# Kernel optimization log

Hardware: AMD Instinct MI355X
Metric: run time of the kernel (lower is better)

The kernel has to match this reference:

```python
import jax, jax.numpy as jnp
import numpy as np

B, T, N, E = 4, 12, 2000, 32000
ND, ED = 16, 8
H, D = 4, 16
G = H * D          # gat_hidden = 64
GH = 64            # gru_hidden
LN_EPS = 1e-5


def setup_inputs() -> dict:
    key = jax.random.key(0)
    ks = jax.random.split(key, 12)

    def xavier(k, shape):
        fan_in, fan_out = shape[0], shape[-1]
        lim = np.sqrt(6.0 / (fan_in + fan_out))
        return jax.random.uniform(k, shape, jnp.float32, -lim, lim)

    return {
        "node_features": jax.random.normal(ks[0], (B, T, N, ND), jnp.float32),
        "edge_features": jax.random.normal(ks[1], (B, T, E, ED), jnp.float32),
        "W_node": xavier(ks[2], (ND, G)),
        "W_edge": xavier(ks[3], (ED, G)),
        "att": xavier(ks[4], (H, 3 * D)),
        "ln_gamma": jnp.ones((G,), jnp.float32),
        "ln_beta": jnp.zeros((G,), jnp.float32),
        "W_ih": xavier(ks[5], (3 * GH, G)),
        "W_hh": xavier(ks[6], (3 * GH, GH)),
        "b_ih": jnp.zeros((3 * GH,), jnp.float32),
        "b_hh": jnp.zeros((3 * GH,), jnp.float32),
        "W_out": xavier(ks[7], (GH, 1)),
        "b_out": jnp.zeros((1,), jnp.float32),
        "edge_index": jax.random.randint(ks[8], (2, E), 0, N).astype(jnp.int64),
    }


def reference(node_features, edge_features, W_node, W_edge, att, ln_gamma,
              ln_beta, W_ih, W_hh, b_ih, b_hh, W_out, b_out, edge_index):
    Bv, Tv, Nv, _ = node_features.shape
    Ev = edge_features.shape[2]
    Hv = att.shape[0]
    Dv = att.shape[1] // 3
    Gv = Hv * Dv
    src, dst = edge_index[0], edge_index[1]
    a_dst, a_src, a_e = att[:, :Dv], att[:, Dv:2 * Dv], att[:, 2 * Dv:]

    def gat_single(x, ea):
        # x: [N, ND], ea: [E, ED]
        h = (x @ W_node).reshape(Nv, Hv, Dv)          # [N,H,D]
        e = (ea @ W_edge).reshape(Ev, Hv, Dv)          # [E,H,D]
        # score = LeakyReLU(a . [h_dst | h_src | e]) — compute per-node parts
        # at node level then gather (same math, avoids [E,H,3D] concat).
        s_d = jnp.einsum('nhd,hd->nh', h, a_dst)       # [N,H]
        s_s = jnp.einsum('nhd,hd->nh', h, a_src)       # [N,H]
        s_e = jnp.einsum('ehd,hd->eh', e, a_e)         # [E,H]
        score = jax.nn.leaky_relu(s_d[dst] + s_s[src] + s_e, 0.2)  # [E,H]
        # segment softmax over in-neighbours of dst
        smax = jax.ops.segment_max(score, dst, num_segments=Nv)
        exp_s = jnp.exp(score - smax[dst])
        ssum = jax.ops.segment_sum(exp_s, dst, num_segments=Nv)
        alpha = exp_s / (ssum[dst] + 1e-16)            # [E,H]
        msg = h[src] + e                               # [E,H,D]
        out = jax.ops.segment_sum(alpha[..., None] * msg, dst,
                                  num_segments=Nv)     # [N,H,D]
        out = jax.nn.elu(out).reshape(Nv, Gv)
        mu = out.mean(-1, keepdims=True)
        var = ((out - mu) ** 2).mean(-1, keepdims=True)
        out = (out - mu) / jnp.sqrt(var + LN_EPS) * ln_gamma + ln_beta
        return out, alpha

    # vmap over the B*T independent graph instances
    x_flat = node_features.reshape(Bv * Tv, Nv, -1)
    e_flat = edge_features.reshape(Bv * Tv, Ev, -1)
    gat_out, alpha_all = jax.vmap(gat_single)(x_flat, e_flat)
    spatial = gat_out.reshape(Bv, Tv, Nv, Gv)
    attn_stack = alpha_all.reshape(Bv, Tv, Ev, Hv).mean(axis=0)  # [T,E,H]

    # GRU over T (batch_first, single layer)
    gru_in = spatial.transpose(0, 2, 1, 3).reshape(Bv * Nv, Tv, Gv)
    xs = gru_in.transpose(1, 0, 2)  # [T, B*N, G]

    def gru_step(hprev, x):
        gi = x @ W_ih.T + b_ih
        gh = hprev @ W_hh.T + b_hh
        i_r, i_z, i_n = jnp.split(gi, 3, axis=-1)
        h_r, h_z, h_n = jnp.split(gh, 3, axis=-1)
        r = jax.nn.sigmoid(i_r + h_r)
        z = jax.nn.sigmoid(i_z + h_z)
        n = jnp.tanh(i_n + r * h_n)
        hnew = (1.0 - z) * n + z * hprev
        return hnew, None

    h0 = jnp.zeros((Bv * Nv, W_hh.shape[1]), gru_in.dtype)
    h_last, _ = jax.lax.scan(gru_step, h0, xs)
    h_i = h_last.reshape(Bv, Nv, -1)               # [B,N,GH]
    pred = h_i @ W_out + b_out                     # [B,N,1]
    return pred, h_i, attn_stack
```

## Files before the change

kernel.cpp:

```cpp
#include <hip/hip_runtime.h>
#include <hip/hip_bf16.h>
#include <math.h>
#include <stdint.h>

#define BQ 4
#define TQ 12
#define NQ 2000
#define EQ 32000
#define NDQ 16
#define EDQ 8
#define HQ 4
#define DQ 16
#define GQ 64
#define GHQ 64
#define NGQ 48
#define LN_EPSQ 1e-5f
#define CCAP 64

typedef _Float16 half8 __attribute__((ext_vector_type(8)));
typedef _Float16 half4v __attribute__((ext_vector_type(4)));
typedef float f32x4 __attribute__((ext_vector_type(4)));

__global__ void k_count(const int* __restrict__ ei, int* __restrict__ count) {
    int e = blockIdx.x * blockDim.x + threadIdx.x;
    if (e < EQ) atomicAdd(&count[ei[EQ + e]], 1);
}

__global__ void k_scan(const int* __restrict__ count, int* __restrict__ offs,
                       int* __restrict__ cursor) {
    __shared__ int buf[2][2048];
    int t = threadIdx.x;
    for (int i = t; i < 2048; i += 1024)
        buf[0][i] = (i < NQ) ? count[i] : 0;
    __syncthreads();
    int src = 0;
    for (int sh = 1; sh < 2048; sh <<= 1) {
        int dst = src ^ 1;
        for (int i = t; i < 2048; i += 1024) {
            int v = buf[src][i];
            if (i >= sh) v += buf[src][i - sh];
            buf[dst][i] = v;
        }
        __syncthreads();
        src = dst;
    }
    for (int i = t; i <= NQ; i += 1024) {
        int off = (i == 0) ? 0 : buf[src][i - 1];
        offs[i] = off;
        if (i < NQ) cursor[i] = off;
    }
}

__global__ void k_scatter(const int* __restrict__ ei, int* __restrict__ cursor,
                          int2* __restrict__ csr2) {
    int e = blockIdx.x * blockDim.x + threadIdx.x;
    if (e < EQ) {
        int pos = atomicAdd(&cursor[ei[EQ + e]], 1);
        csr2[pos] = make_int2(e, ei[e]);
    }
}

__global__ void k_nodeproj(const float* __restrict__ xf, const float* __restrict__ Wn,
                           const float* __restrict__ att,
                           _Float16* __restrict__ hprojH, float* __restrict__ sd,
                           float* __restrict__ ss) {
    __shared__ float Wl[NDQ * GQ];
    int t = threadIdx.x;
    for (int i = t; i < NDQ * GQ; i += blockDim.x) Wl[i] = Wn[i];
    __syncthreads();
    int wid = (blockIdx.x * blockDim.x + t) >> 6;
    int lane = t & 63;
    int g = wid / NQ, n = wid % NQ;
    const float* x = xf + ((size_t)g * NQ + n) * NDQ;
    float acc = 0.f;
#pragma unroll
    for (int i = 0; i < NDQ; ++i) acc = fmaf(x[i], Wl[i * GQ + lane], acc);
    hprojH[((size_t)g * NQ + n) * GQ + lane] = (_Float16)acc;
    int hh = lane >> 4, d = lane & 15;
    float vd = acc * att[hh * 48 + d];
    float vs = acc * att[hh * 48 + 16 + d];
#pragma unroll
    for (int s = 8; s >= 1; s >>= 1) {
        vd += __shfl_xor(vd, s, 64);
        vs += __shfl_xor(vs, s, 64);
    }
    if (d == 0) {
        sd[((size_t)g * NQ + n) * HQ + hh] = vd;
        ss[((size_t)g * NQ + n) * HQ + hh] = vs;
    }
}

__global__ void __launch_bounds__(256) k_fused(
        const float* __restrict__ ef, const float* __restrict__ We,
        const float* __restrict__ att,
        const int* __restrict__ offs, const int2* __restrict__ csr2,
        const float* __restrict__ sd, const float* __restrict__ ss,
        const _Float16* __restrict__ hprojH,
        const float* __restrict__ gamma, const float* __restrict__ beta,
        _Float16* __restrict__ alphaH, _Float16* __restrict__ spatialH) {
    __shared__ float Wl[EDQ * GQ];
    __shared__ __align__(16) float WA[EDQ * HQ];
    __shared__ __align__(16) float ecache[4][CCAP * 4];
    __shared__ half8 eac[4][CCAP];
    __shared__ int   srcs[4][CCAP];
    __shared__ int   eids[4][CCAP];
    int t = threadIdx.x;
    for (int i = t; i < EDQ * GQ; i += 256) Wl[i] = We[i];
    if (t < EDQ * HQ) {
        int i = t >> 2, h4 = t & 3;
        float s = 0.f;
#pragma unroll
        for (int d = 0; d < DQ; ++d)
            s = fmaf(We[i * GQ + h4 * DQ + d], att[h4 * 48 + 32 + d], s);
        WA[t] = s;
    }
    __syncthreads();
    int w = t >> 6, lane = t & 63;
    int wid = blockIdx.x * 4 + w;
    int g = wid / NQ, n = wid % NQ;
    int beg = offs[n], deg = offs[n + 1] - beg;
    size_t ebase = (size_t)g * EQ;
    size_t nbase = (size_t)g * NQ;
    float4 sd4 = *(const float4*)&sd[(nbase + n) * HQ];
    float mxr[4] = {-1e30f, -1e30f, -1e30f, -1e30f};
    for (int k = lane; k < deg; k += 64) {
        int2 pr = csr2[beg + k];
        float4 ssv = *(const float4*)&ss[(nbase + pr.y) * HQ];
        const float4* eap = (const float4*)(ef + (ebase + pr.x) * EDQ);
        float4 lo = eap[0], hi = eap[1];
        float scv[4];
#pragma unroll
        for (int hh = 0; hh < 4; ++hh) {
            float4 w0 = *(const float4*)&WA[0 * 4];
            float se;
            {
                se =            lo.x * WA[0 * 4 + hh];
                se = fmaf(lo.y, WA[1 * 4 + hh], se);
                se = fmaf(lo.z, WA[2 * 4 + hh], se);
                se = fmaf(lo.w, WA[3 * 4 + hh], se);
                se = fmaf(hi.x, WA[4 * 4 + hh], se);
                se = fmaf(hi.y, WA[5 * 4 + hh], se);
                se = fmaf(hi.z, WA[6 * 4 + hh], se);
                se = fmaf(hi.w, WA[7 * 4 + hh], se);
            }
            (void)w0;
            float sdh = (hh == 0) ? sd4.x : (hh == 1) ? sd4.y : (hh == 2) ? sd4.z : sd4.w;
            float ssh = (hh == 0) ? ssv.x : (hh == 1) ? ssv.y : (hh == 2) ? ssv.z : ssv.w;
            float sc = sdh + ssh + se;
            sc = (sc >= 0.f) ? sc : 0.2f * sc;
            scv[hh] = sc;
            mxr[hh] = fmaxf(mxr[hh], sc);
        }
        if (k < CCAP) {
            *(float4*)&ecache[w][k * 4] = make_float4(scv[0], scv[1], scv[2], scv[3]);
            half8 hv;
            hv[0] = (_Float16)lo.x; hv[1] = (_Float16)lo.y;
            hv[2] = (_Float16)lo.z; hv[3] = (_Float16)lo.w;
            hv[4] = (_Float16)hi.x; hv[5] = (_Float16)hi.y;
            hv[6] = (_Float16)hi.z; hv[7] = (_Float16)hi.w;
            eac[w][k] = hv;
            srcs[w][k] = pr.y;
            eids[w][k] = pr.x;
        }
    }
#pragma unroll
    for (int s = 1; s < 64; s <<= 1) {
#pragma unroll
        for (int hh = 0; hh < 4; ++hh)
            mxr[hh] = fmaxf(mxr[hh], __shfl_xor(mxr[hh], s, 64));
    }
    int h = lane >> 4, c = lane & 15;
    float mxh = (h == 0) ? mxr[0] : (h == 1) ? mxr[1] : (h == 2) ? mxr[2] : mxr[3];
    float sdh = (h == 0) ? sd4.x : (h == 1) ? sd4.y : (h == 2) ? sd4.z : sd4.w;
    float sum = 0.f;
    float ws[8] = {0.f, 0.f, 0.f, 0.f, 0.f, 0.f, 0.f, 0.f};
    for (int k = c; k < deg; k += 16) {
        float e;
        if (k < CCAP) {
            e = __expf(ecache[w][k * 4 + h] - mxh);
            ecache[w][k * 4 + h] = e;
            half8 ev = eac[w][k];
#pragma unroll
            for (int i = 0; i < 8; ++i) ws[i] = fmaf(e, (float)ev[i], ws[i]);
        } else {
            int2 pr = csr2[beg + k];
            float4 ssv = *(const float4*)&ss[(nbase + pr.y) * HQ];
            float ssh = (h == 0) ? ssv.x : (h == 1) ? ssv.y : (h == 2) ? ssv.z : ssv.w;
            const float4* eap = (const float4*)(ef + (ebase + pr.x) * EDQ);
            float4 lo = eap[0], hi = eap[1];
            float se =      lo.x * WA[0 * 4 + h];
            se = fmaf(lo.y, WA[1 * 4 + h], se); se = fmaf(lo.z, WA[2 * 4 + h], se);
            se = fmaf(lo.w, WA[3 * 4 + h], se); se = fmaf(hi.x, WA[4 * 4 + h], se);
            se = fmaf(hi.y, WA[5 * 4 + h], se); se = fmaf(hi.z, WA[6 * 4 + h], se);
            se = fmaf(hi.w, WA[7 * 4 + h], se);
            float sc = sdh + ssh + se;
            sc = (sc >= 0.f) ? sc : 0.2f * sc;
            e = __expf(sc - mxh);
            ws[0] = fmaf(e, lo.x, ws[0]); ws[1] = fmaf(e, lo.y, ws[1]);
            ws[2] = fmaf(e, lo.z, ws[2]); ws[3] = fmaf(e, lo.w, ws[3]);
            ws[4] = fmaf(e, hi.x, ws[4]); ws[5] = fmaf(e, hi.y, ws[5]);
            ws[6] = fmaf(e, hi.z, ws[6]); ws[7] = fmaf(e, hi.w, ws[7]);
        }
        sum += e;
    }
#pragma unroll
    for (int s = 1; s < 16; s <<= 1) {
        sum += __shfl_xor(sum, s, 16);
#pragma unroll
        for (int i = 0; i < 8; ++i) ws[i] += __shfl_xor(ws[i], s, 16);
    }
    float inv = 1.f / (sum + 1e-16f);
#pragma unroll
    for (int i = 0; i < 8; ++i) ws[i] *= inv;
    for (int k = c; k < deg; k += 16) {
        float e; int eid;
        if (k < CCAP) {
            e = ecache[w][k * 4 + h];
            eid = eids[w][k];
        } else {
            int2 pr = csr2[beg + k];
            eid = pr.x;
            float4 ssv = *(const float4*)&ss[(nbase + pr.y) * HQ];
            float ssh = (h == 0) ? ssv.x : (h == 1) ? ssv.y : (h == 2) ? ssv.z : ssv.w;
            const float4* eap = (const float4*)(ef + (ebase + pr.x) * EDQ);
            float4 lo = eap[0], hi = eap[1];
            float se =      lo.x * WA[0 * 4 + h];
            se = fmaf(lo.y, WA[1 * 4 + h], se); se = fmaf(lo.z, WA[2 * 4 + h], se);
            se = fmaf(lo.w, WA[3 * 4 + h], se); se = fmaf(hi.x, WA[4 * 4 + h], se);
            se = fmaf(hi.y, WA[5 * 4 + h], se); se = fmaf(hi.z, WA[6 * 4 + h], se);
            se = fmaf(hi.w, WA[7 * 4 + h], se);
            float sc = sdh + ssh + se;
            sc = (sc >= 0.f) ? sc : 0.2f * sc;
            e = __expf(sc - mxh);
        }
        alphaH[(ebase + eid) * HQ + h] = (_Float16)(e * inv);
    }
    int dmain = deg < CCAP ? deg : CCAP;
    float acc = 0.f;
    int k = 0;
    for (; k + 4 <= dmain; k += 4) {
        float e0 = ecache[w][(k + 0) * 4 + h];
        float e1 = ecache[w][(k + 1) * 4 + h];
        float e2 = ecache[w][(k + 2) * 4 + h];
        float e3 = ecache[w][(k + 3) * 4 + h];
        int s0 = srcs[w][k + 0], s1 = srcs[w][k + 1];
        int s2 = srcs[w][k + 2], s3 = srcs[w][k + 3];
        float h0 = (float)hprojH[(nbase + s0) * GQ + lane];
        float h1 = (float)hprojH[(nbase + s1) * GQ + lane];
        float h2 = (float)hprojH[(nbase + s2) * GQ + lane];
        float h3 = (float)hprojH[(nbase + s3) * GQ + lane];
        acc = fmaf(e0, h0, acc); acc = fmaf(e1, h1, acc);
        acc = fmaf(e2, h2, acc); acc = fmaf(e3, h3, acc);
    }
    for (; k < dmain; ++k) {
        float e0 = ecache[w][k * 4 + h];
        float h0 = (float)hprojH[(nbase + srcs[w][k]) * GQ + lane];
        acc = fmaf(e0, h0, acc);
    }
    for (; k < deg; ++k) {
        int2 pr = csr2[beg + k];
        float4 ssv = *(const float4*)&ss[(nbase + pr.y) * HQ];
        float ssh = (h == 0) ? ssv.x : (h == 1) ? ssv.y : (h == 2) ? ssv.z : ssv.w;
        const float4* eap = (const float4*)(ef + (ebase + pr.x) * EDQ);
        float4 lo = eap[0], hi = eap[1];
        float se =      lo.x * WA[0 * 4 + h];
        se = fmaf(lo.y, WA[1 * 4 + h], se); se = fmaf(lo.z, WA[2 * 4 + h], se);
        se = fmaf(lo.w, WA[3 * 4 + h], se); se = fmaf(hi.x, WA[4 * 4 + h], se);
        se = fmaf(hi.y, WA[5 * 4 + h], se); se = fmaf(hi.z, WA[6 * 4 + h], se);
        se = fmaf(hi.w, WA[7 * 4 + h], se);
        float sc = sdh + ssh + se;
        sc = (sc >= 0.f) ? sc : 0.2f * sc;
        float e0 = __expf(sc - mxh);
        float h0 = (float)hprojH[(nbase + pr.y) * GQ + lane];
        acc = fmaf(e0, h0, acc);
    }
    acc *= inv;
    float t2 = 0.f;
#pragma unroll
    for (int i = 0; i < 8; ++i) t2 = fmaf(ws[i], Wl[i * GQ + lane], t2);
    float x = acc + t2;
    x = (x > 0.f) ? x : (__expf(x) - 1.f);
    float s1 = x, s2v = x * x;
#pragma unroll
    for (int s = 32; s >= 1; s >>= 1) {
        s1 += __shfl_xor(s1, s, 64);
        s2v += __shfl_xor(s2v, s, 64);
    }
    float mu = s1 * (1.f / 64.f);
    float var = s2v * (1.f / 64.f) - mu * mu;
    float y = (x - mu) * rsqrtf(var + LN_EPSQ) * gamma[lane] + beta[lane];
    spatialH[(nbase + n) * GQ + lane] = (_Float16)y;
}

__device__ inline f32x4 MF(half8 a, half8 b, f32x4 c) {
    return __builtin_amdgcn_mfma_f32_16x16x32_f16(a, b, c, 0, 0, 0);
}

__global__ void __launch_bounds__(256) k_gru(
        const _Float16* __restrict__ xh,
        const float* __restrict__ Wih, const float* __restrict__ Whh,
        const float* __restrict__ bih, const float* __restrict__ bhh,
        const float* __restrict__ Wout, const float* __restrict__ bout,
        float* __restrict__ out) {
    __shared__ _Float16 hlds[32][72];
    __shared__ float pred_s[4][32];
    int tid = threadIdx.x;
    int w = tid >> 6, l = tid & 63;
    int lr = l & 15, lg = l >> 4;
    int j = w * 16 + lr;
    half8 wiF[3][2], whF[3][2];
#pragma unroll
    for (int gb = 0; gb < 3; ++gb) {
        int q = gb * 64 + j;
#pragma unroll
        for (int kt = 0; kt < 2; ++kt) {
            const float* p  = Wih + q * 64 + kt * 32 + lg * 8;
            const float* p2 = Whh + q * 64 + kt * 32 + lg * 8;
            half8 a, b;
#pragma unroll
            for (int i = 0; i < 8; ++i) { a[i] = (_Float16)p[i]; b[i] = (_Float16)p2[i]; }
            wiF[gb][kt] = a; whF[gb][kt] = b;
        }
    }
    float br  = bih[j] + bhh[j];
    float bz  = bih[64 + j] + bhh[64 + j];
    float bin = bih[128 + j];
    float bhn = bhh[128 + j];
    float wo  = Wout[j];
    for (int i = tid; i < 32 * 72; i += 256) ((_Float16*)hlds)[i] = (_Float16)0.f;
    int id0 = blockIdx.x * 32;
    const _Float16* xp0; const _Float16* xp1;
    {
        int id = id0 + lr;          int b = id / NQ, n = id - b * NQ;
        xp0 = xh + ((size_t)b * TQ * NQ + n) * GQ + lg * 8;
        int id2 = id0 + 16 + lr;    int b2 = id2 / NQ, n2 = id2 - b2 * NQ;
        xp1 = xh + ((size_t)b2 * TQ * NQ + n2) * GQ + lg * 8;
    }
    half8 xa[2][2];
    xa[0][0] = *(const half8*)xp0; xa[0][1] = *(const half8*)(xp0 + 32);
    xa[1][0] = *(const half8*)xp1; xa[1][1] = *(const half8*)(xp1 + 32);
    float hprev[2][4] = {{0.f,0.f,0.f,0.f},{0.f,0.f,0.f,0.f}};
    __syncthreads();
    for (int t = 0; t < TQ; ++t) {
        f32x4 aR[2], aZ[2], aIN[2], aHN[2];
#pragma unroll
        for (int mt = 0; mt < 2; ++mt) {
            aR[mt]  = (f32x4){br, br, br, br};
            aZ[mt]  = (f32x4){bz, bz, bz, bz};
            aIN[mt] = (f32x4){bin, bin, bin, bin};
            aHN[mt] = (f32x4){bhn, bhn, bhn, bhn};
        }
#pragma unroll
        for (int mt = 0; mt < 2; ++mt)
#pragma unroll
            for (int kt = 0; kt < 2; ++kt) {
                aR[mt]  = MF(xa[mt][kt], wiF[0][kt], aR[mt]);
                aZ[mt]  = MF(xa[mt][kt], wiF[1][kt], aZ[mt]);
                aIN[mt] = MF(xa[mt][kt], wiF[2][kt], aIN[mt]);
            }
        half8 ha[2][2];
#pragma unroll
        for (int mt = 0; mt < 2; ++mt) {
            ha[mt][0] = *(const half8*)&hlds[16 * mt + lr][lg * 8];
            ha[mt][1] = *(const half8*)&hlds[16 * mt + lr][32 + lg * 8];
        }
#pragma unroll
        for (int mt = 0; mt < 2; ++mt)
#pragma unroll
            for (int kt = 0; kt < 2; ++kt) {
                aR[mt]  = MF(ha[mt][kt], whF[0][kt], aR[mt]);
                aZ[mt]  = MF(ha[mt][kt], whF[1][kt], aZ[mt]);
                aHN[mt] = MF(ha[mt][kt], whF[2][kt], aHN[mt]);
            }
        if (t + 1 < TQ) {
            xp0 += (size_t)NQ * GQ; xp1 += (size_t)NQ * GQ;
            xa[0][0] = *(const half8*)xp0; xa[0][1] = *(const half8*)(xp0 + 32);
            xa[1][0] = *(const half8*)xp1; xa[1][1] = *(const half8*)(xp1 + 32);
        }
#pragma unroll
        for (int mt = 0; mt < 2; ++mt)
#pragma unroll
            for (int r4 = 0; r4 < 4; ++r4) {
                float r = 1.f / (1.f + __expf(-aR[mt][r4]));
                float z = 1.f / (1.f + __expf(-aZ[mt][r4]));
                float xg = aIN[mt][r4] + r * aHN[mt][r4];
                float e2 = __expf(2.f * xg);
                float nn = 1.f - 2.f / (e2 + 1.f);
                hprev[mt][r4] = z * (hprev[mt][r4] - nn) + nn;
            }
        __syncthreads();
#pragma unroll
        for (int mt = 0; mt < 2; ++mt)
#pragma unroll
            for (int r4 = 0; r4 < 4; ++r4)
                hlds[16 * mt + 4 * lg + r4][j] = (_Float16)hprev[mt][r4];
        __syncthreads();
    }
    float pv[2][4];
#pragma unroll
    for (int mt = 0; mt < 2; ++mt)
#pragma unroll
        for (int r4 = 0; r4 < 4; ++r4) {
            int id = id0 + 16 * mt + 4 * lg + r4;
            out[8000 + (size_t)id * GHQ + j] = hprev[mt][r4];
            pv[mt][r4] = hprev[mt][r4] * wo;
        }
#pragma unroll
    for (int s = 1; s <= 8; s <<= 1)
#pragma unroll
        for (int mt = 0; mt < 2; ++mt)
#pragma unroll
            for (int r4 = 0; r4 < 4; ++r4)
                pv[mt][r4] += __shfl_xor(pv[mt][r4], s);
    if (lr == 0) {
#pragma unroll
        for (int mt = 0; mt < 2; ++mt)
#pragma unroll
            for (int r4 = 0; r4 < 4; ++r4)
                pred_s[w][16 * mt + 4 * lg + r4] = pv[mt][r4];
    }
    __syncthreads();
    if (tid < 32) {
        float s = pred_s[0][tid] + pred_s[1][tid] + pred_s[2][tid] + pred_s[3][tid] + bout[0];
        out[id0 + tid] = s;
    }
}

__global__ void k_attn(const _Float16* __restrict__ alpha, float* __restrict__ out) {
    int gid = blockIdx.x * blockDim.x + threadIdx.x;
    if (gid >= TQ * EQ) return;
    int tt = gid / EQ, e = gid % EQ;
    float a0 = 0.f, a1 = 0.f, a2 = 0.f, a3 = 0.f;
#pragma unroll
    for (int b = 0; b < BQ; ++b) {
        half4v v = *(const half4v*)&alpha[(((size_t)b * TQ + tt) * EQ + e) * HQ];
        a0 += (float)v[0]; a1 += (float)v[1]; a2 += (float)v[2]; a3 += (float)v[3];
    }
    float4 r = {a0 * 0.25f, a1 * 0.25f, a2 * 0.25f, a3 * 0.25f};
    *(float4*)&out[520000 + (size_t)gid * HQ] = r;
}

extern "C" void kernel_launch(void* const* d_in, const int* in_sizes, int n_in,
                              void* d_out, int out_size, void* d_ws, size_t ws_size,
                              hipStream_t stream) {
    const float* nodef = (const float*)d_in[0];
    const float* edgef = (const float*)d_in[1];
    const float* Wn    = (const float*)d_in[2];
    const float* We    = (const float*)d_in[3];
    const float* att   = (const float*)d_in[4];
    const float* gamma = (const float*)d_in[5];
    const float* beta  = (const float*)d_in[6];
    const float* Wih   = (const float*)d_in[7];
    const float* Whh   = (const float*)d_in[8];
    const float* bih   = (const float*)d_in[9];
    const float* bhh   = (const float*)d_in[10];
    const float* Wout  = (const float*)d_in[11];
    const float* bout  = (const float*)d_in[12];
    const int*   ei    = (const int*)d_in[13];

    char* ws = (char*)d_ws;
    size_t o = 0;
    int*  count  = (int*)(ws + o);  o += 2048 * 4;
    int*  offs   = (int*)(ws + o);  o += 2048 * 4;
    int*  cursor = (int*)(ws + o);  o += 2048 * 4;
    int2* csr2   = (int2*)(ws + o); o += (size_t)EQ * 8;
    float* sd      = (float*)(ws + o); o += (size_t)NGQ * NQ * HQ * 4;
    float* ss      = (float*)(ws + o); o += (size_t)NGQ * NQ * HQ * 4;
    _Float16* hprojH   = (_Float16*)(ws + o); o += (size_t)NGQ * NQ * GQ * 2;
    _Float16* alphaH   = (_Float16*)(ws + o); o += (size_t)NGQ * EQ * HQ * 2;
    _Float16* spatialH = (_Float16*)(ws + o); o += (size_t)NGQ * NQ * GQ * 2;

    hipMemsetAsync(count, 0, NQ * sizeof(int), stream);
    k_count  <<<(EQ + 255) / 256, 256, 0, stream>>>(ei, count);
    k_scan   <<<1, 1024, 0, stream>>>(count, offs, cursor);
    k_scatter<<<(EQ + 255) / 256, 256, 0, stream>>>(ei, cursor, csr2);

    k_nodeproj<<<(NGQ * NQ * 64) / 256, 256, 0, stream>>>(nodef, Wn, att, hprojH, sd, ss);
    k_fused   <<<(NGQ * NQ) / 4, 256, 0, stream>>>(edgef, We, att, offs, csr2,
                                                   sd, ss, hprojH, gamma, beta,
                                                   alphaH, spatialH);
    k_gru     <<<(BQ * NQ) / 32, 256, 0, stream>>>(spatialH, Wih, Whh, bih, bhh,
                                                   Wout, bout, (float*)d_out);
    k_attn    <<<(TQ * EQ + 255) / 256, 256, 0, stream>>>(alphaH, (float*)d_out);
}
```

Baseline: 297.4 us.

## Fuse attention averaging into GAT via atomics, restructure nodeproj and GRU tiling

Removes the fp16 alpha buffer and the k_attn kernel. The fused GAT kernel now atomically adds 0.25*alpha straight into the output attention region, which is zeroed beforehand with a memset, and it processes all four heads per lane. k_nodeproj switches from one wave per node to one thread per node with a register-held 64-wide accumulator and vectorized stores. The GRU kernel is retiled from 32 to 16 rows per block, doubling the block count. The aggregation loop is also unrolled to 8. Atomic float adds make the result order nondeterministic and add atomic traffic, and nodeproj now needs many more registers per thread.

```diff
diff --git a/kernel.cpp b/kernel.cpp
--- a/kernel.cpp
+++ b/kernel.cpp
@@ -16,9 +16,9 @@
 #define NGQ 48
 #define LN_EPSQ 1e-5f
 #define CCAP 64
+#define ATTN_OFF 520000
 
 typedef _Float16 half8 __attribute__((ext_vector_type(8)));
-typedef _Float16 half4v __attribute__((ext_vector_type(4)));
 typedef float f32x4 __attribute__((ext_vector_type(4)));
 
 __global__ void k_count(const int* __restrict__ ei, int* __restrict__ count) {
@@ -60,33 +60,56 @@
     }
 }
 
-__global__ void k_nodeproj(const float* __restrict__ xf, const float* __restrict__ Wn,
-                           const float* __restrict__ att,
-                           _Float16* __restrict__ hprojH, float* __restrict__ sd,
-                           float* __restrict__ ss) {
-    __shared__ float Wl[NDQ * GQ];
+__global__ void __launch_bounds__(256) k_nodeproj(
+        const float* __restrict__ xf, const float* __restrict__ Wn,
+        const float* __restrict__ att,
+        _Float16* __restrict__ hprojH, float* __restrict__ sd,
+        float* __restrict__ ss) {
+    __shared__ __align__(16) float4 Wl4[NDQ * 16];
+    __shared__ float attl[HQ * 48];
     int t = threadIdx.x;
-    for (int i = t; i < NDQ * GQ; i += blockDim.x) Wl[i] = Wn[i];
+    for (int i = t; i < NDQ * 16; i += 256) Wl4[i] = ((const float4*)Wn)[i];
+    if (t < HQ * 48) attl[t] = att[t];
     __syncthreads();
-    int wid = (blockIdx.x * blockDim.x + t) >> 6;
-    int lane = t & 63;
-    int g = wid / NQ, n = wid % NQ;
-    const float* x = xf + ((size_t)g * NQ + n) * NDQ;
-    float acc = 0.f;
-#pragma unroll
-    for (int i = 0; i < NDQ; ++i) acc = fmaf(x[i], Wl[i * GQ + lane], acc);
-    hprojH[((size_t)g * NQ + n) * GQ + lane] = (_Float16)acc;
-    int hh = lane >> 4, d = lane & 15;
-    float vd = acc * att[hh * 48 + d];
-    float vs = acc * att[hh * 48 + 16 + d];
-#pragma unroll
-    for (int s = 8; s >= 1; s >>= 1) {
-        vd += __shfl_xor(vd, s, 64);
-        vs += __shfl_xor(vs, s, 64);
-    }
-    if (d == 0) {
-        sd[((size_t)g * NQ + n) * HQ + hh] = vd;
-        ss[((size_t)g * NQ + n) * HQ + hh] = vs;
+    int id = blockIdx.x * 256 + t;
+    const float4* xp = (const float4*)(xf + (size_t)id * NDQ);
+    float4 xv0 = xp[0], xv1 = xp[1], xv2 = xp[2], xv3 = xp[3];
+    float xr[16] = {xv0.x, xv0.y, xv0.z, xv0.w, xv1.x, xv1.y, xv1.z, xv1.w,
+                    xv2.x, xv2.y, xv2.z, xv2.w, xv3.x, xv3.y, xv3.z, xv3.w};
+    float acc[64];
+#pragma unroll
+    for (int j = 0; j < 64; ++j) acc[j] = 0.f;
+#pragma unroll
+    for (int i = 0; i < 16; ++i) {
+        float xi = xr[i];
+#pragma unroll
+        for (int j4 = 0; j4 < 16; ++j4) {
+            float4 wv = Wl4[i * 16 + j4];
+            acc[j4 * 4 + 0] = fmaf(xi, wv.x, acc[j4 * 4 + 0]);
+            acc[j4 * 4 + 1] = fmaf(xi, wv.y, acc[j4 * 4 + 1]);
+            acc[j4 * 4 + 2] = fmaf(xi, wv.z, acc[j4 * 4 + 2]);
+            acc[j4 * 4 + 3] = fmaf(xi, wv.w, acc[j4 * 4 + 3]);
+        }
+    }
+    float sdv[4], ssv[4];
+#pragma unroll
+    for (int hh = 0; hh < 4; ++hh) {
+        float vd = 0.f, vs = 0.f;
+#pragma unroll
+        for (int d = 0; d < 16; ++d) {
+            vd = fmaf(acc[hh * 16 + d], attl[hh * 48 + d], vd);
+            vs = fmaf(acc[hh * 16 + d], attl[hh * 48 + 16 + d], vs);
+        }
+        sdv[hh] = vd; ssv[hh] = vs;
+    }
+    *(float4*)&sd[(size_t)id * 4] = make_float4(sdv[0], sdv[1], sdv[2], sdv[3]);
+    *(float4*)&ss[(size_t)id * 4] = make_float4(ssv[0], ssv[1], ssv[2], ssv[3]);
+#pragma unroll
+    for (int p = 0; p < 8; ++p) {
+        half8 hv;
+#pragma unroll
+        for (int i = 0; i < 8; ++i) hv[i] = (_Float16)acc[p * 8 + i];
+        *(half8*)&hprojH[(size_t)id * GQ + p * 8] = hv;
     }
 }
 
@@ -97,7 +120,7 @@
         const float* __restrict__ sd, const float* __restrict__ ss,
         const _Float16* __restrict__ hprojH,
         const float* __restrict__ gamma, const float* __restrict__ beta,
-        _Float16* __restrict__ alphaH, _Float16* __restrict__ spatialH) {
+        float* __restrict__ outAttn, _Float16* __restrict__ spatialH) {
     __shared__ float Wl[EDQ * GQ];
     __shared__ __align__(16) float WA[EDQ * HQ];
     __shared__ __align__(16) float ecache[4][CCAP * 4];
@@ -131,19 +154,11 @@
         float scv[4];
 #pragma unroll
         for (int hh = 0; hh < 4; ++hh) {
-            float4 w0 = *(const float4*)&WA[0 * 4];
-            float se;
-            {
-                se =            lo.x * WA[0 * 4 + hh];
-                se = fmaf(lo.y, WA[1 * 4 + hh], se);
-                se = fmaf(lo.z, WA[2 * 4 + hh], se);
-                se = fmaf(lo.w, WA[3 * 4 + hh], se);
-                se = fmaf(hi.x, WA[4 * 4 + hh], se);
-                se = fmaf(hi.y, WA[5 * 4 + hh], se);
-                se = fmaf(hi.z, WA[6 * 4 + hh], se);
-                se = fmaf(hi.w, WA[7 * 4 + hh], se);
-            }
-            (void)w0;
+            float se =      lo.x * WA[0 * 4 + hh];
+            se = fmaf(lo.y, WA[1 * 4 + hh], se); se = fmaf(lo.z, WA[2 * 4 + hh], se);
+            se = fmaf(lo.w, WA[3 * 4 + hh], se); se = fmaf(hi.x, WA[4 * 4 + hh], se);
+            se = fmaf(hi.y, WA[5 * 4 + hh], se); se = fmaf(hi.z, WA[6 * 4 + hh], se);
+            se = fmaf(hi.w, WA[7 * 4 + hh], se);
             float sdh = (hh == 0) ? sd4.x : (hh == 1) ? sd4.y : (hh == 2) ? sd4.z : sd4.w;
             float ssh = (hh == 0) ? ssv.x : (hh == 1) ? ssv.y : (hh == 2) ? ssv.z : ssv.w;
             float sc = sdh + ssh + se;
@@ -212,49 +227,66 @@
     float inv = 1.f / (sum + 1e-16f);
 #pragma unroll
     for (int i = 0; i < 8; ++i) ws[i] *= inv;
-    for (int k = c; k < deg; k += 16) {
-        float e; int eid;
+    float inv4[4];
+#pragma unroll
+    for (int hh = 0; hh < 4; ++hh) inv4[hh] = __shfl(inv, hh * 16, 64);
+    int tt = g % TQ;
+    float* aout = outAttn + ATTN_OFF + (size_t)tt * EQ * HQ;
+    for (int k = lane; k < deg; k += 64) {
+        float e4[4]; int eid;
         if (k < CCAP) {
-            e = ecache[w][k * 4 + h];
             eid = eids[w][k];
+            float4 ev = *(const float4*)&ecache[w][k * 4];
+            e4[0] = ev.x; e4[1] = ev.y; e4[2] = ev.z; e4[3] = ev.w;
         } else {
             int2 pr = csr2[beg + k];
             eid = pr.x;
             float4 ssv = *(const float4*)&ss[(nbase + pr.y) * HQ];
-            float ssh = (h == 0) ? ssv.x : (h == 1) ? ssv.y : (h == 2) ? ssv.z : ssv.w;
             const float4* eap = (const float4*)(ef + (ebase + pr.x) * EDQ);
             float4 lo = eap[0], hi = eap[1];
-            float se =      lo.x * WA[0 * 4 + h];
-            se = fmaf(lo.y, WA[1 * 4 + h], se); se = fmaf(lo.z, WA[2 * 4 + h], se);
-            se = fmaf(lo.w, WA[3 * 4 + h], se); se = fmaf(hi.x, WA[4 * 4 + h], se);
-            se = fmaf(hi.y, WA[5 * 4 + h], se); se = fmaf(hi.z, WA[6 * 4 + h], se);
-            se = fmaf(hi.w, WA[7 * 4 + h], se);
-            float sc = sdh + ssh + se;
-            sc = (sc >= 0.f) ? sc : 0.2f * sc;
-            e = __expf(sc - mxh);
-        }
-        alphaH[(ebase + eid) * HQ + h] = (_Float16)(e * inv);
+#pragma unroll
+            for (int hh = 0; hh < 4; ++hh) {
+                float se =      lo.x * WA[0 * 4 + hh];
+                se = fmaf(lo.y, WA[1 * 4 + hh], se); se = fmaf(lo.z, WA[2 * 4 + hh], se);
+                se = fmaf(lo.w, WA[3 * 4 + hh], se); se = fmaf(hi.x, WA[4 * 4 + hh], se);
+                se = fmaf(hi.y, WA[5 * 4 + hh], se); se = fmaf(hi.z, WA[6 * 4 + hh], se);
+                se = fmaf(hi.w, WA[7 * 4 + hh], se);
+                float sdh2 = (hh == 0) ? sd4.x : (hh == 1) ? sd4.y : (hh == 2) ? sd4.z : sd4.w;
+                float ssh2 = (hh == 0) ? ssv.x : (hh == 1) ? ssv.y : (hh == 2) ? ssv.z : ssv.w;
+                float sc = sdh2 + ssh2 + se;
+                sc = (sc >= 0.f) ? sc : 0.2f * sc;
+                e4[hh] = __expf(sc - mxr[hh]);
+            }
+        }
+#pragma unroll
+        for (int hh = 0; hh < 4; ++hh)
+            atomicAdd(&aout[(size_t)eid * HQ + hh], 0.25f * e4[hh] * inv4[hh]);
     }
     int dmain = deg < CCAP ? deg : CCAP;
+    const _Float16* hp = hprojH + nbase * GQ + lane;
     float acc = 0.f;
     int k = 0;
-    for (; k + 4 <= dmain; k += 4) {
-        float e0 = ecache[w][(k + 0) * 4 + h];
-        float e1 = ecache[w][(k + 1) * 4 + h];
-        float e2 = ecache[w][(k + 2) * 4 + h];
-        float e3 = ecache[w][(k + 3) * 4 + h];
-        int s0 = srcs[w][k + 0], s1 = srcs[w][k + 1];
-        int s2 = srcs[w][k + 2], s3 = srcs[w][k + 3];
-        float h0 = (float)hprojH[(nbase + s0) * GQ + lane];
-        float h1 = (float)hprojH[(nbase + s1) * GQ + lane];
-        float h2 = (float)hprojH[(nbase + s2) * GQ + lane];
-        float h3 = (float)hprojH[(nbase + s3) * GQ + lane];
+    for (; k + 8 <= dmain; k += 8) {
+        float e0 = ecache[w][(k + 0) * 4 + h], e1 = ecache[w][(k + 1) * 4 + h];
+        float e2 = ecache[w][(k + 2) * 4 + h], e3 = ecache[w][(k + 3) * 4 + h];
+        float e4 = ecache[w][(k + 4) * 4 + h], e5 = ecache[w][(k + 5) * 4 + h];
+        float e6 = ecache[w][(k + 6) * 4 + h], e7 = ecache[w][(k + 7) * 4 + h];
+        float h0 = (float)hp[(size_t)srcs[w][k + 0] * GQ];
+        float h1 = (float)hp[(size_t)srcs[w][k + 1] * GQ];
+        float h2 = (float)hp[(size_t)srcs[w][k + 2] * GQ];
+        float h3 = (float)hp[(size_t)srcs[w][k + 3] * GQ];
+        float h4 = (float)hp[(size_t)srcs[w][k + 4] * GQ];
+        float h5 = (float)hp[(size_t)srcs[w][k + 5] * GQ];
+        float h6 = (float)hp[(size_t)srcs[w][k + 6] * GQ];
+        float h7 = (float)hp[(size_t)srcs[w][k + 7] * GQ];
         acc = fmaf(e0, h0, acc); acc = fmaf(e1, h1, acc);
         acc = fmaf(e2, h2, acc); acc = fmaf(e3, h3, acc);
+        acc = fmaf(e4, h4, acc); acc = fmaf(e5, h5, acc);
+        acc = fmaf(e6, h6, acc); acc = fmaf(e7, h7, acc);
     }
     for (; k < dmain; ++k) {
         float e0 = ecache[w][k * 4 + h];
-        float h0 = (float)hprojH[(nbase + srcs[w][k]) * GQ + lane];
+        float h0 = (float)hp[(size_t)srcs[w][k] * GQ];
         acc = fmaf(e0, h0, acc);
     }
     for (; k < deg; ++k) {
@@ -271,7 +303,7 @@
         float sc = sdh + ssh + se;
         sc = (sc >= 0.f) ? sc : 0.2f * sc;
         float e0 = __expf(sc - mxh);
-        float h0 = (float)hprojH[(nbase + pr.y) * GQ + lane];
+        float h0 = (float)hp[(size_t)pr.y * GQ];
         acc = fmaf(e0, h0, acc);
     }
     acc *= inv;
@@ -302,8 +334,8 @@
         const float* __restrict__ bih, const float* __restrict__ bhh,
         const float* __restrict__ Wout, const float* __restrict__ bout,
         float* __restrict__ out) {
-    __shared__ _Float16 hlds[32][72];
-    __shared__ float pred_s[4][32];
+    __shared__ _Float16 hlds[16][72];
+    __shared__ float pred_s[4][16];
     int tid = threadIdx.x;
     int w = tid >> 6, l = tid & 63;
     int lr = l & 15, lg = l >> 4;
@@ -327,117 +359,79 @@
     float bin = bih[128 + j];
     float bhn = bhh[128 + j];
     float wo  = Wout[j];
-    for (int i = tid; i < 32 * 72; i += 256) ((_Float16*)hlds)[i] = (_Float16)0.f;
-    int id0 = blockIdx.x * 32;
-    const _Float16* xp0; const _Float16* xp1;
+    for (int i = tid; i < 16 * 72; i += 256) ((_Float16*)hlds)[i] = (_Float16)0.f;
+    int id0 = blockIdx.x * 16;
+    const _Float16* xp0;
     {
-        int id = id0 + lr;          int b = id / NQ, n = id - b * NQ;
+        int id = id0 + lr;
+        int b = id / NQ, n = id - b * NQ;
         xp0 = xh + ((size_t)b * TQ * NQ + n) * GQ + lg * 8;
-        int id2 = id0 + 16 + lr;    int b2 = id2 / NQ, n2 = id2 - b2 * NQ;
-        xp1 = xh + ((size_t)b2 * TQ * NQ + n2) * GQ + lg * 8;
-    }
-    half8 xa[2][2];
-    xa[0][0] = *(const half8*)xp0; xa[0][1] = *(const half8*)(xp0 + 32);
-    xa[1][0] = *(const half8*)xp1; xa[1][1] = *(const half8*)(xp1 + 32);
-    float hprev[2][4] = {{0.f,0.f,0.f,0.f},{0.f,0.f,0.f,0.f}};
+    }
+    half8 xa[2];
+    xa[0] = *(const half8*)xp0; xa[1] = *(const half8*)(xp0 + 32);
+    float hprev[4] = {0.f, 0.f, 0.f, 0.f};
     __syncthreads();
     for (int t = 0; t < TQ; ++t) {
-        f32x4 aR[2], aZ[2], aIN[2], aHN[2];
-#pragma unroll
-        for (int mt = 0; mt < 2; ++mt) {
-            aR[mt]  = (f32x4){br, br, br, br};
-            aZ[mt]  = (f32x4){bz, bz, bz, bz};
-            aIN[mt] = (f32x4){bin, bin, bin, bin};
-            aHN[mt] = (f32x4){bhn, bhn, bhn, bhn};
-        }
-#pragma unroll
-        for (int mt = 0; mt < 2; ++mt)
-#pragma unroll
-            for (int kt = 0; kt < 2; ++kt) {
-                aR[mt]  = MF(xa[mt][kt], wiF[0][kt], aR[mt]);
-                aZ[mt]  = MF(xa[mt][kt], wiF[1][kt], aZ[mt]);
-                aIN[mt] = MF(xa[mt][kt], wiF[2][kt], aIN[mt]);
-            }
-        half8 ha[2][2];
-#pragma unroll
-        for (int mt = 0; mt < 2; ++mt) {
-            ha[mt][0] = *(const half8*)&hlds[16 * mt + lr][lg * 8];
-            ha[mt][1] = *(const half8*)&hlds[16 * mt + lr][32 + lg * 8];
-        }
-#pragma unroll
-        for (int mt = 0; mt < 2; ++mt)
-#pragma unroll
-            for (int kt = 0; kt < 2; ++kt) {
-                aR[mt]  = MF(ha[mt][kt], whF[0][kt], aR[mt]);
-                aZ[mt]  = MF(ha[mt][kt], whF[1][kt], aZ[mt]);
-                aHN[mt] = MF(ha[mt][kt], whF[2][kt], aHN[mt]);
-            }
+        f32x4 aR  = (f32x4){br, br, br, br};
+        f32x4 aZ  = (f32x4){bz, bz, bz, bz};
+        f32x4 aIN = (f32x4){bin, bin, bin, bin};
+        f32x4 aHN = (f32x4){bhn, bhn, bhn, bhn};
+#pragma unroll
+        for (int kt = 0; kt < 2; ++kt) {
+            aR  = MF(xa[kt], wiF[0][kt], aR);
+            aZ  = MF(xa[kt], wiF[1][kt], aZ);
+            aIN = MF(xa[kt], wiF[2][kt], aIN);
+        }
+        half8 ha[2];
+        ha[0] = *(const half8*)&hlds[lr][lg * 8];
+        ha[1] = *(const half8*)&hlds[lr][32 + lg * 8];
+#pragma unroll
+        for (int kt = 0; kt < 2; ++kt) {
+            aR  = MF(ha[kt], whF[0][kt], aR);
+            aZ  = MF(ha[kt], whF[1][kt], aZ);
+            aHN = MF(ha[kt], whF[2][kt], aHN);
+        }
         if (t + 1 < TQ) {
-            xp0 += (size_t)NQ * GQ; xp1 += (size_t)NQ * GQ;
-            xa[0][0] = *(const half8*)xp0; xa[0][1] = *(const half8*)(xp0 + 32);
-            xa[1][0] = *(const half8*)xp1; xa[1][1] = *(const half8*)(xp1 + 32);
-        }
-#pragma unroll
-        for (int mt = 0; mt < 2; ++mt)
-#pragma unroll
-            for (int r4 = 0; r4 < 4; ++r4) {
-                float r = 1.f / (1.f + __expf(-aR[mt][r4]));
-                float z = 1.f / (1.f + __expf(-aZ[mt][r4]));
-                float xg = aIN[mt][r4] + r * aHN[mt][r4];
-                float e2 = __expf(2.f * xg);
-                float nn = 1.f - 2.f / (e2 + 1.f);
-                hprev[mt][r4] = z * (hprev[mt][r4] - nn) + nn;
-            }
+            xp0 += (size_t)NQ * GQ;
+            xa[0] = *(const half8*)xp0; xa[1] = *(const half8*)(xp0 + 32);
+        }
+#pragma unroll
+        for (int r4 = 0; r4 < 4; ++r4) {
+            float r = 1.f / (1.f + __expf(-aR[r4]));
+            float z = 1.f / (1.f + __expf(-aZ[r4]));
+            float xg = aIN[r4] + r * aHN[r4];
+            float e2 = __expf(2.f * xg);
+            float nn = 1.f - 2.f / (e2 + 1.f);
+            hprev[r4] = z * (hprev[r4] - nn) + nn;
+        }
         __syncthreads();
 #pragma unroll
-        for (int mt = 0; mt < 2; ++mt)
-#pragma unroll
-            for (int r4 = 0; r4 < 4; ++r4)
-                hlds[16 * mt + 4 * lg + r4][j] = (_Float16)hprev[mt][r4];
+        for (int r4 = 0; r4 < 4; ++r4)
+            hlds[4 * lg + r4][j] = (_Float16)hprev[r4];
         __syncthreads();
     }
-    float pv[2][4];
-#pragma unroll
-    for (int mt = 0; mt < 2; ++mt)
-#pragma unroll
-        for (int r4 = 0; r4 < 4; ++r4) {
-            int id = id0 + 16 * mt + 4 * lg + r4;
-            out[8000 + (size_t)id * GHQ + j] = hprev[mt][r4];
-            pv[mt][r4] = hprev[mt][r4] * wo;
-        }
+    float pv[4];
+#pragma unroll
+    for (int r4 = 0; r4 < 4; ++r4) {
+        int id = id0 + 4 * lg + r4;
+        out[8000 + (size_t)id * GHQ + j] = hprev[r4];
+        pv[r4] = hprev[r4] * wo;
+    }
 #pragma unroll
     for (int s = 1; s <= 8; s <<= 1)
 #pragma unroll
-        for (int mt = 0; mt < 2; ++mt)
-#pragma unroll
-            for (int r4 = 0; r4 < 4; ++r4)
-                pv[mt][r4] += __shfl_xor(pv[mt][r4], s);
+        for (int r4 = 0; r4 < 4; ++r4)
+            pv[r4] += __shfl_xor(pv[r4], s);
     if (lr == 0) {
 #pragma unroll
-        for (int mt = 0; mt < 2; ++mt)
-#pragma unroll
-            for (int r4 = 0; r4 < 4; ++r4)
-                pred_s[w][16 * mt + 4 * lg + r4] = pv[mt][r4];
+        for (int r4 = 0; r4 < 4; ++r4)
+            pred_s[w][4 * lg + r4] = pv[r4];
     }
     __syncthreads();
-    if (tid < 32) {
+    if (tid < 16) {
         float s = pred_s[0][tid] + pred_s[1][tid] + pred_s[2][tid] + pred_s[3][tid] + bout[0];
         out[id0 + tid] = s;
     }
-}
-
-__global__ void k_attn(const _Float16* __restrict__ alpha, float* __restrict__ out) {
-    int gid = blockIdx.x * blockDim.x + threadIdx.x;
-    if (gid >= TQ * EQ) return;
-    int tt = gid / EQ, e = gid % EQ;
-    float a0 = 0.f, a1 = 0.f, a2 = 0.f, a3 = 0.f;
-#pragma unroll
-    for (int b = 0; b < BQ; ++b) {
-        half4v v = *(const half4v*)&alpha[(((size_t)b * TQ + tt) * EQ + e) * HQ];
-        a0 += (float)v[0]; a1 += (float)v[1]; a2 += (float)v[2]; a3 += (float)v[3];
-    }
-    float4 r = {a0 * 0.25f, a1 * 0.25f, a2 * 0.25f, a3 * 0.25f};
-    *(float4*)&out[520000 + (size_t)gid * HQ] = r;
 }
 
 extern "C" void kernel_launch(void* const* d_in, const int* in_sizes, int n_in,
@@ -467,19 +461,18 @@
     float* sd      = (float*)(ws + o); o += (size_t)NGQ * NQ * HQ * 4;
     float* ss      = (float*)(ws + o); o += (size_t)NGQ * NQ * HQ * 4;
     _Float16* hprojH   = (_Float16*)(ws + o); o += (size_t)NGQ * NQ * GQ * 2;
-    _Float16* alphaH   = (_Float16*)(ws + o); o += (size_t)NGQ * EQ * HQ * 2;
     _Float16* spatialH = (_Float16*)(ws + o); o += (size_t)NGQ * NQ * GQ * 2;
 
     hipMemsetAsync(count, 0, NQ * sizeof(int), stream);
+    hipMemsetAsync((float*)d_out + ATTN_OFF, 0, (size_t)TQ * EQ * HQ * 4, stream);
     k_count  <<<(EQ + 255) / 256, 256, 0, stream>>>(ei, count);
     k_scan   <<<1, 1024, 0, stream>>>(count, offs, cursor);
     k_scatter<<<(EQ + 255) / 256, 256, 0, stream>>>(ei, cursor, csr2);
 
-    k_nodeproj<<<(NGQ * NQ * 64) / 256, 256, 0, stream>>>(nodef, Wn, att, hprojH, sd, ss);
+    k_nodeproj<<<(NGQ * NQ) / 256, 256, 0, stream>>>(nodef, Wn, att, hprojH, sd, ss);
     k_fused   <<<(NGQ * NQ) / 4, 256, 0, stream>>>(edgef, We, att, offs, csr2,
                                                    sd, ss, hprojH, gamma, beta,
-                                                   alphaH, spatialH);
-    k_gru     <<<(BQ * NQ) / 32, 256, 0, stream>>>(spatialH, Wih, Whh, bih, bhh,
+                                                   (float*)d_out, spatialH);
+    k_gru     <<<(BQ * NQ) / 16, 256, 0, stream>>>(spatialH, Wih, Whh, bih, bhh,
                                                    Wout, bout, (float*)d_out);
-    k_attn    <<<(TQ * EQ + 255) / 256, 256, 0, stream>>>(alphaH, (float*)d_out);
-}
+}
```

New measurement: 474.0 us. 59.4% more time.
